# Performance work log

Hardware: AMD Instinct MI355X
Metric: run time of the kernel (lower is better)

## Reference

```python
import jax, jax.numpy as jnp
import numpy as np


def log_g(x):
    # log of g(x) = x + 0.5 for x>=0, sigmoid(x) for x<0
    return jnp.where(x >= 0, jnp.log(jax.nn.relu(x) + 0.5), -jax.nn.softplus(-x))


def setup_inputs() -> dict:
    key = jax.random.key(0)
    k1, k2 = jax.random.split(key)
    B, S, D = 4, 4096, 1024
    x = jax.random.normal(k1, (B, S, D), dtype=jnp.float32)
    # nn.Linear(dim, 2*dim, bias=False) weight: [2*dim, dim], scaled like kaiming-uniform-ish
    W = jax.random.normal(k2, (2 * D, D), dtype=jnp.float32) * (1.0 / np.sqrt(D))
    return {"x": x, "W": W}


def reference(x, W):
    # x: [B, S, D], W: [2D, D] -> hidden, gate: [B, S, D]
    hg = jnp.einsum("bsd,ed->bse", x, W)
    hidden, gate = jnp.split(hg, 2, axis=-1)

    log_coeffs = -jax.nn.softplus(gate)        # log(1 - z)
    log_z = -jax.nn.softplus(-gate)            # log(z)
    log_values = log_z + log_g(hidden)

    # Heinsen associative scan in log space along seq axis
    a_star = jnp.cumsum(log_coeffs, axis=1)
    log_h0_plus_b_star = jax.lax.cumlogsumexp(log_values - a_star, axis=1)
    log_h = a_star + log_h0_plus_b_star
    out = jnp.exp(log_h)                       # [B, S, D]
    # expansion_factor == 1.0 -> to_out is Identity
    return out
```

## Files before the change

kernel.cpp:

```cpp
#include <hip/hip_runtime.h>
#include <hip/hip_bf16.h>
#include <hip/hip_fp16.h>
#include <math.h>
#include <string.h>

#define B_  4
#define S_  4096
#define D_  1024
#define M_  (B_ * S_)
#define K_  D_
#define L_  32
#define NC_ (S_ / L_)
#define NKT 16

typedef __attribute__((ext_vector_type(8))) short          bf16x8;
typedef __attribute__((ext_vector_type(8))) unsigned short u16x8;
typedef __attribute__((ext_vector_type(4))) float          f32x4;

__device__ __forceinline__ unsigned short f2bf(float f) {
    union { __hip_bfloat16 h; unsigned short u; } cv;
    cv.h = __float2bfloat16(f);
    return cv.u;
}

__device__ __forceinline__ float fast_rcp(float x) {
#if __has_builtin(__builtin_amdgcn_rcpf)
    return __builtin_amdgcn_rcpf(x);
#else
    return 1.0f / x;
#endif
}

__device__ __forceinline__ void stage16(const unsigned short* src, char* dst) {
    __builtin_amdgcn_global_load_lds(
        (const __attribute__((address_space(1))) unsigned int*)src,
        (__attribute__((address_space(3))) unsigned int*)dst, 16, 0, 0);
}

__global__ __launch_bounds__(256) void to_bf16_both(
    const float* __restrict__ x, const float* __restrict__ W,
    unsigned short* __restrict__ xb, unsigned short* __restrict__ Wb,
    int n8x, int n8w)
{
    int i = blockIdx.x * 256 + threadIdx.x;
    const float* src;
    unsigned short* dst;
    int j;
    if (i < n8x) { src = x; dst = xb; j = i; }
    else {
        j = i - n8x;
        if (j >= n8w) return;
        src = W; dst = Wb;
    }
    const float4* p = (const float4*)src + (size_t)j * 2;
    float4 a = p[0], b = p[1];
    u16x8 o;
    o[0] = f2bf(a.x); o[1] = f2bf(a.y); o[2] = f2bf(a.z); o[3] = f2bf(a.w);
    o[4] = f2bf(b.x); o[5] = f2bf(b.y); o[6] = f2bf(b.z); o[7] = f2bf(b.w);
    *(u16x8*)(dst + (size_t)j * 8) = o;
}

__global__ __launch_bounds__(512, 2) void gemm_pointwise(
    const unsigned short* __restrict__ xb, const unsigned short* __restrict__ Wb,
    __half2* __restrict__ cvb, float2* __restrict__ CVagg)
{
    __shared__ char lds[131072];

    const int th   = threadIdx.x;
    const int lane = th & 63;
    const int wave = th >> 6;
    const int wm = wave >> 2;
    const int wn = wave & 3;

    const int wg  = blockIdx.x;
    const int swz = (wg & 7) * 64 + (wg >> 3);
    const int m0 = (swz >> 3) * 256;
    const int d0 = (swz & 7) * 128;

    f32x4 acc[8][4];
#pragma unroll
    for (int i = 0; i < 8; ++i)
#pragma unroll
        for (int j = 0; j < 4; ++j)
            acc[i][j] = (f32x4){0.f, 0.f, 0.f, 0.f};

    const int srow = th >> 2;
    const int scol = (((th & 3) ^ ((th >> 3) & 3)) * 8);
    const unsigned short* srcA  = xb + (size_t)(m0 + srow)       * K_ + scol;
    const unsigned short* srcA2 = xb + (size_t)(m0 + 128 + srow) * K_ + scol;
    const unsigned short* srcBh = Wb + (size_t)(d0 + srow)       * K_ + scol;
    const unsigned short* srcBg = Wb + (size_t)(D_ + d0 + srow)  * K_ + scol;
    char* const wuo = lds + wave * 1024;

    const int lr = lane & 15;
    const int lq = lane >> 4;
    const int lkb = ((lq ^ ((lr >> 1) & 3)) * 16);
    const int aoffb = (wm * 128 + lr) * 64 + lkb;
    const int boffb = 32768 + (wn * 32 + lr) * 64 + lkb;

    bf16x8 Aa[4], Ab[4], Ba[4], Bb[4];

#define BAR()  asm volatile("s_barrier" ::: "memory")
#define LGK0() asm volatile("s_waitcnt lgkmcnt(0)" ::: "memory")
#define VM0()  asm volatile("s_waitcnt vmcnt(0)" ::: "memory")

#define CLUSTER(base, AF, BF) do {                                        \
    __builtin_amdgcn_s_setprio(1);                                        \
    _Pragma("unroll")                                                     \
    for (int i_ = 0; i_ < 4; ++i_)                                        \
        _Pragma("unroll")                                                 \
        for (int j_ = 0; j_ < 4; ++j_)                                    \
            acc[(base) + i_][j_] = __builtin_amdgcn_mfma_f32_16x16x32_bf16(\
                AF[i_], BF[j_], acc[(base) + i_][j_], 0, 0, 0);           \
    __builtin_amdgcn_s_setprio(0);                                        \
  } while (0)

    stage16(srcA,       wuo + 0);
    stage16(srcA2,      wuo + 8192);
    stage16(srcA  + 32, wuo + 16384);
    stage16(srcA2 + 32, wuo + 24576);
    stage16(srcBh,      wuo + 32768);
    stage16(srcBg,      wuo + 40960);
    stage16(srcBh + 32, wuo + 49152);
    stage16(srcBg + 32, wuo + 57344);
    VM0();
    BAR();
    {
        const char* bc = lds;
#pragma unroll
        for (int i = 0; i < 4; ++i)
            Aa[i] = *(const bf16x8*)(bc + aoffb + i * 1024);
#pragma unroll
        for (int j = 0; j < 2; ++j) {
            Ba[j]     = *(const bf16x8*)(bc + boffb + j * 1024);
            Ba[j + 2] = *(const bf16x8*)(bc + boffb + 8192 + j * 1024);
        }
    }

#pragma unroll 1
    for (int t = 0; t < NKT; ++t) {
        const char* bc  = lds + (t & 1) * 65536;
        char*       bn  = wuo + ((t + 1) & 1) * 65536;
        const char* bnr = lds + ((t + 1) & 1) * 65536;
        const int kof = (t + 1) * 64;
        const bool pre = (t < NKT - 1);

#pragma unroll
        for (int i = 0; i < 4; ++i)
            Ab[i] = *(const bf16x8*)(bc + aoffb + 4096 + i * 1024);
        if (pre) {
            stage16(srcA  + kof,      bn + 0);
            stage16(srcA2 + kof,      bn + 8192);
            stage16(srcA  + kof + 32, bn + 16384);
            stage16(srcA2 + kof + 32, bn + 24576);
        }
        BAR(); LGK0();
        CLUSTER(0, Aa, Ba);
        BAR();

#pragma unroll
        for (int i = 0; i < 4; ++i)
            Aa[i] = *(const bf16x8*)(bc + aoffb + 16384 + i * 1024);
#pragma unroll
        for (int j = 0; j < 2; ++j) {
            Bb[j]     = *(const bf16x8*)(bc + boffb + 16384 + j * 1024);
            Bb[j + 2] = *(const bf16x8*)(bc + boffb + 16384 + 8192 + j * 1024);
        }
        if (pre) {
            stage16(srcBh + kof,      bn + 32768);
            stage16(srcBg + kof,      bn + 40960);
            stage16(srcBh + kof + 32, bn + 49152);
            stage16(srcBg + kof + 32, bn + 57344);
        }
        BAR(); LGK0();
        CLUSTER(4, Ab, Ba);
        BAR();

#pragma unroll
        for (int i = 0; i < 4; ++i)
            Ab[i] = *(const bf16x8*)(bc + aoffb + 4096 + 16384 + i * 1024);
        BAR(); LGK0();
        CLUSTER(0, Aa, Bb);
        BAR();

        VM0();
        BAR();
        if (pre) {
#pragma unroll
            for (int i = 0; i < 4; ++i)
                Aa[i] = *(const bf16x8*)(bnr + aoffb + i * 1024);
#pragma unroll
            for (int j = 0; j < 2; ++j) {
                Ba[j]     = *(const bf16x8*)(bnr + boffb + j * 1024);
                Ba[j + 2] = *(const bf16x8*)(bnr + boffb + 8192 + j * 1024);
            }
        }
        CLUSTER(4, Ab, Bb);
    }
#undef CLUSTER
#undef BAR
#undef LGK0
#undef VM0

#pragma unroll
    for (int mp = 0; mp < 4; ++mp) {
        float C16[2][2], V16[2][2];
#pragma unroll
        for (int hf = 0; hf < 2; ++hf) {
            const int mi = mp * 2 + hf;
#pragma unroll
            for (int nj = 0; nj < 2; ++nj) {
                float C4 = 1.0f, V4 = 0.0f;
                const int d = d0 + wn * 32 + nj * 16 + lr;
#pragma unroll
                for (int r = 0; r < 4; ++r) {
                    int m = m0 + wm * 128 + mi * 16 + lq * 4 + r;
                    float h = acc[mi][nj][r];
                    float g = acc[mi][nj + 2][r];
                    float eg  = __expf(g);
                    float c   = fast_rcp(1.0f + eg);
                    float z   = eg * c;
                    float enh = __expf(-h);
                    float sh  = fast_rcp(1.0f + enh);
                    float gh  = (h >= 0.0f) ? (h + 0.5f) : sh;
                    float v   = z * gh;
                    cvb[(size_t)m * D_ + d] = __floats2half2_rn(c, v);
                    V4 = fmaf(c, V4, v);
                    C4 *= c;
                }
                float Ca = __shfl_xor(C4, 16), Va = __shfl_xor(V4, 16);
                float Clo = (lq & 1) ? Ca : C4, Vlo = (lq & 1) ? Va : V4;
                float Chi = (lq & 1) ? C4 : Ca, Vhi = (lq & 1) ? V4 : Va;
                float C2 = Clo * Chi, V2 = fmaf(Chi, Vlo, Vhi);
                float Cb = __shfl_xor(C2, 32), Vb = __shfl_xor(V2, 32);
                float Cl2 = (lq & 2) ? Cb : C2, Vl2 = (lq & 2) ? Vb : V2;
                float Ch2 = (lq & 2) ? C2 : Cb, Vh2 = (lq & 2) ? V2 : Vb;
                C16[hf][nj] = Cl2 * Ch2;
                V16[hf][nj] = fmaf(Ch2, Vl2, Vh2);
            }
        }
        if (lq == 0) {
            const int chunkg = (m0 + wm * 128 + mp * 32) >> 5;
#pragma unroll
            for (int nj = 0; nj < 2; ++nj) {
                float C32 = C16[0][nj] * C16[1][nj];
                float V32 = fmaf(C16[1][nj], V16[0][nj], V16[1][nj]);
                const int d = d0 + wn * 32 + nj * 16 + lr;
                float2 st; st.x = C32; st.y = V32;
                CVagg[(size_t)chunkg * D_ + d] = st;
            }
        }
    }
}

__global__ __launch_bounds__(256) void chunk_scan(
    const float2* __restrict__ CVagg, float* __restrict__ P)
{
    const int d = blockIdx.x * 256 + threadIdx.x;
    const int b = blockIdx.z;
    float h = 0.0f;
    for (int c = 0; c < NC_; ++c) {
        size_t o = ((size_t)b * NC_ + c) * D_ + d;
        P[o] = h;
        float2 cv = CVagg[o];
        h = fmaf(cv.x, h, cv.y);
    }
}

__global__ __launch_bounds__(256) void chunk_apply(
    const unsigned long long* __restrict__ cvw,
    const float* __restrict__ P, float* __restrict__ out)
{
    const int d = (blockIdx.x * 256 + threadIdx.x) * 2;
    const int c = blockIdx.y;
    const int b = blockIdx.z;
    size_t base2 = (((size_t)(b * S_ + c * L_)) * D_ + d) >> 1;
    float2 h2 = *(const float2*)(P + ((size_t)b * NC_ + c) * D_ + d);
    float h0 = h2.x, h1 = h2.y;
    unsigned long long* outp = (unsigned long long*)out;
    union Cvt { unsigned long long ull; uint2 u2; float2 f2; };
#pragma unroll
    for (int s = 0; s < L_; ++s) {
        Cvt in;
        in.ull = __builtin_nontemporal_load(cvw + base2 + (size_t)s * (D_ / 2));
        float2 p0 = __half22float2(*(const __half2*)&in.u2.x);
        float2 p1 = __half22float2(*(const __half2*)&in.u2.y);
        h0 = fmaf(p0.x, h0, p0.y);
        h1 = fmaf(p1.x, h1, p1.y);
        Cvt o;
        o.f2.x = h0; o.f2.y = h1;
        __builtin_nontemporal_store(o.ull, outp + base2 + (size_t)s * (D_ / 2));
    }
}

extern "C" void kernel_launch(void* const* d_in, const int* in_sizes, int n_in,
                              void* d_out, int out_size, void* d_ws, size_t ws_size,
                              hipStream_t stream) {
    const float* x = (const float*)d_in[0];
    const float* W = (const float*)d_in[1];
    float* out = (float*)d_out;

    float2* CVagg = (float2*)d_ws;
    float*  P     = (float*)(CVagg + (size_t)B_ * NC_ * D_);
    __half2* cvb  = (__half2*)(P + (size_t)B_ * NC_ * D_);
    unsigned short* xb = (unsigned short*)(cvb + (size_t)M_ * D_);
    unsigned short* Wb = xb + (size_t)M_ * K_;

    const int n8x = M_ * K_ / 8;
    const int n8w = 2 * D_ * K_ / 8;
    to_bf16_both<<<(n8x + n8w + 255) / 256, 256, 0, stream>>>(x, W, xb, Wb, n8x, n8w);

    gemm_pointwise<<<512, 512, 0, stream>>>(xb, Wb, cvb, CVagg);

    dim3 g3(D_ / 256, 1, B_);
    chunk_scan<<<g3, 256, 0, stream>>>(CVagg, P);

    dim3 g2(D_ / 512, NC_, B_);
    chunk_apply<<<g2, 256, 0, stream>>>((const unsigned long long*)cvb, P, out);
}
```

Measured before the change: 123.8 us.

## Fuse x fp32-to-bf16 conversion into GEMM A-tile loading via registers

After: 126.3 us. +2.0%, slower.

```diff
diff --git a/kernel.cpp b/kernel.cpp
--- a/kernel.cpp
+++ b/kernel.cpp
@@ -2,7 +2,6 @@
 #include <hip/hip_bf16.h>
 #include <hip/hip_fp16.h>
 #include <math.h>
-#include <string.h>
 
 #define B_  4
 #define S_  4096
@@ -37,31 +36,21 @@
         (__attribute__((address_space(3))) unsigned int*)dst, 16, 0, 0);
 }
 
-__global__ __launch_bounds__(256) void to_bf16_both(
-    const float* __restrict__ x, const float* __restrict__ W,
-    unsigned short* __restrict__ xb, unsigned short* __restrict__ Wb,
-    int n8x, int n8w)
+__global__ __launch_bounds__(256) void to_bf16(
+    const float* __restrict__ in, unsigned short* __restrict__ out, int n8)
 {
     int i = blockIdx.x * 256 + threadIdx.x;
-    const float* src;
-    unsigned short* dst;
-    int j;
-    if (i < n8x) { src = x; dst = xb; j = i; }
-    else {
-        j = i - n8x;
-        if (j >= n8w) return;
-        src = W; dst = Wb;
-    }
-    const float4* p = (const float4*)src + (size_t)j * 2;
+    if (i >= n8) return;
+    const float4* p = (const float4*)in + (size_t)i * 2;
     float4 a = p[0], b = p[1];
     u16x8 o;
     o[0] = f2bf(a.x); o[1] = f2bf(a.y); o[2] = f2bf(a.z); o[3] = f2bf(a.w);
     o[4] = f2bf(b.x); o[5] = f2bf(b.y); o[6] = f2bf(b.z); o[7] = f2bf(b.w);
-    *(u16x8*)(dst + (size_t)j * 8) = o;
+    *(u16x8*)(out + (size_t)i * 8) = o;
 }
 
 __global__ __launch_bounds__(512, 2) void gemm_pointwise(
-    const unsigned short* __restrict__ xb, const unsigned short* __restrict__ Wb,
+    const float* __restrict__ xf, const unsigned short* __restrict__ Wb,
     __half2* __restrict__ cvb, float2* __restrict__ CVagg)
 {
     __shared__ char lds[131072];
@@ -86,11 +75,12 @@
 
     const int srow = th >> 2;
     const int scol = (((th & 3) ^ ((th >> 3) & 3)) * 8);
-    const unsigned short* srcA  = xb + (size_t)(m0 + srow)       * K_ + scol;
-    const unsigned short* srcA2 = xb + (size_t)(m0 + 128 + srow) * K_ + scol;
-    const unsigned short* srcBh = Wb + (size_t)(d0 + srow)       * K_ + scol;
-    const unsigned short* srcBg = Wb + (size_t)(D_ + d0 + srow)  * K_ + scol;
+    const float*          srcAf  = xf + (size_t)(m0 + srow)       * K_ + scol;
+    const float*          srcAf2 = xf + (size_t)(m0 + 128 + srow) * K_ + scol;
+    const unsigned short* srcBh  = Wb + (size_t)(d0 + srow)       * K_ + scol;
+    const unsigned short* srcBg  = Wb + (size_t)(D_ + d0 + srow)  * K_ + scol;
     char* const wuo = lds + wave * 1024;
+    const int thb = th * 16;
 
     const int lr = lane & 15;
     const int lq = lane >> 4;
@@ -99,10 +89,39 @@
     const int boffb = 32768 + (wn * 32 + lr) * 64 + lkb;
 
     bf16x8 Aa[4], Ab[4], Ba[4], Bb[4];
+    float4 aL[8];
 
 #define BAR()  asm volatile("s_barrier" ::: "memory")
 #define LGK0() asm volatile("s_waitcnt lgkmcnt(0)" ::: "memory")
 #define VM0()  asm volatile("s_waitcnt vmcnt(0)" ::: "memory")
+
+#define LOAD_A(kof) do {                                                  \
+    const float* s0_ = srcAf  + (kof);                                    \
+    const float* s1_ = srcAf2 + (kof);                                    \
+    aL[0] = *(const float4*)(s0_);      aL[1] = *(const float4*)(s0_ + 4);\
+    aL[2] = *(const float4*)(s1_);      aL[3] = *(const float4*)(s1_ + 4);\
+    aL[4] = *(const float4*)(s0_ + 32); aL[5] = *(const float4*)(s0_ + 36);\
+    aL[6] = *(const float4*)(s1_ + 32); aL[7] = *(const float4*)(s1_ + 36);\
+  } while (0)
+
+#define WRITE_A(dst) do {                                                 \
+    _Pragma("unroll")                                                     \
+    for (int s_ = 0; s_ < 4; ++s_) {                                      \
+        u16x8 o_;                                                         \
+        o_[0] = f2bf(aL[2*s_].x);   o_[1] = f2bf(aL[2*s_].y);             \
+        o_[2] = f2bf(aL[2*s_].z);   o_[3] = f2bf(aL[2*s_].w);             \
+        o_[4] = f2bf(aL[2*s_+1].x); o_[5] = f2bf(aL[2*s_+1].y);           \
+        o_[6] = f2bf(aL[2*s_+1].z); o_[7] = f2bf(aL[2*s_+1].w);           \
+        *(u16x8*)((dst) + s_ * 8192 + thb) = o_;                          \
+    }                                                                     \
+  } while (0)
+
+#define STAGE_B(kof, bufdst) do {                                         \
+    stage16(srcBh + (kof),      (bufdst) + 32768);                        \
+    stage16(srcBg + (kof),      (bufdst) + 40960);                        \
+    stage16(srcBh + (kof) + 32, (bufdst) + 49152);                        \
+    stage16(srcBg + (kof) + 32, (bufdst) + 57344);                        \
+  } while (0)
 
 #define CLUSTER(base, AF, BF) do {                                        \
     __builtin_amdgcn_s_setprio(1);                                        \
@@ -115,15 +134,11 @@
     __builtin_amdgcn_s_setprio(0);                                        \
   } while (0)
 
-    stage16(srcA,       wuo + 0);
-    stage16(srcA2,      wuo + 8192);
-    stage16(srcA  + 32, wuo + 16384);
-    stage16(srcA2 + 32, wuo + 24576);
-    stage16(srcBh,      wuo + 32768);
-    stage16(srcBg,      wuo + 40960);
-    stage16(srcBh + 32, wuo + 49152);
-    stage16(srcBg + 32, wuo + 57344);
+    LOAD_A(0);
+    STAGE_B(0, wuo);
     VM0();
+    WRITE_A(lds);
+    LGK0();
     BAR();
     {
         const char* bc = lds;
@@ -141,6 +156,7 @@
     for (int t = 0; t < NKT; ++t) {
         const char* bc  = lds + (t & 1) * 65536;
         char*       bn  = wuo + ((t + 1) & 1) * 65536;
+        char*       bnw = lds + ((t + 1) & 1) * 65536;
         const char* bnr = lds + ((t + 1) & 1) * 65536;
         const int kof = (t + 1) * 64;
         const bool pre = (t < NKT - 1);
@@ -148,12 +164,7 @@
 #pragma unroll
         for (int i = 0; i < 4; ++i)
             Ab[i] = *(const bf16x8*)(bc + aoffb + 4096 + i * 1024);
-        if (pre) {
-            stage16(srcA  + kof,      bn + 0);
-            stage16(srcA2 + kof,      bn + 8192);
-            stage16(srcA  + kof + 32, bn + 16384);
-            stage16(srcA2 + kof + 32, bn + 24576);
-        }
+        if (pre) { LOAD_A(kof); }
         BAR(); LGK0();
         CLUSTER(0, Aa, Ba);
         BAR();
@@ -166,12 +177,7 @@
             Bb[j]     = *(const bf16x8*)(bc + boffb + 16384 + j * 1024);
             Bb[j + 2] = *(const bf16x8*)(bc + boffb + 16384 + 8192 + j * 1024);
         }
-        if (pre) {
-            stage16(srcBh + kof,      bn + 32768);
-            stage16(srcBg + kof,      bn + 40960);
-            stage16(srcBh + kof + 32, bn + 49152);
-            stage16(srcBg + kof + 32, bn + 57344);
-        }
+        if (pre) { STAGE_B(kof, bn); }
         BAR(); LGK0();
         CLUSTER(4, Ab, Ba);
         BAR();
@@ -184,6 +190,8 @@
         BAR();
 
         VM0();
+        if (pre) { WRITE_A(bnw); }
+        LGK0();
         BAR();
         if (pre) {
 #pragma unroll
@@ -198,6 +206,9 @@
         CLUSTER(4, Ab, Bb);
     }
 #undef CLUSTER
+#undef STAGE_B
+#undef WRITE_A
+#undef LOAD_A
 #undef BAR
 #undef LGK0
 #undef VM0
@@ -303,14 +314,12 @@
     float2* CVagg = (float2*)d_ws;
     float*  P     = (float*)(CVagg + (size_t)B_ * NC_ * D_);
     __half2* cvb  = (__half2*)(P + (size_t)B_ * NC_ * D_);
-    unsigned short* xb = (unsigned short*)(cvb + (size_t)M_ * D_);
-    unsigned short* Wb = xb + (size_t)M_ * K_;
-
-    const int n8x = M_ * K_ / 8;
+    unsigned short* Wb = (unsigned short*)(cvb + (size_t)M_ * D_);
+
     const int n8w = 2 * D_ * K_ / 8;
-    to_bf16_both<<<(n8x + n8w + 255) / 256, 256, 0, stream>>>(x, W, xb, Wb, n8x, n8w);
-
-    gemm_pointwise<<<512, 512, 0, stream>>>(xb, Wb, cvb, CVagg);
+    to_bf16<<<(n8w + 255) / 256, 256, 0, stream>>>(W, Wb, n8w);
+
+    gemm_pointwise<<<512, 512, 0, stream>>>(x, Wb, cvb, CVagg);
 
     dim3 g3(D_ / 256, 1, B_);
     chunk_scan<<<g3, 256, 0, stream>>>(CVagg, P);
```

## Load B fragments directly from global memory, staging only A in LDS

Applied to the files above, without the earlier changes.

Result: slower. 167.1 us (+34.9%).

```diff
diff --git a/kernel.cpp b/kernel.cpp
--- a/kernel.cpp
+++ b/kernel.cpp
@@ -2,7 +2,6 @@
 #include <hip/hip_bf16.h>
 #include <hip/hip_fp16.h>
 #include <math.h>
-#include <string.h>
 
 #define B_  4
 #define S_  4096
@@ -64,7 +63,7 @@
     const unsigned short* __restrict__ xb, const unsigned short* __restrict__ Wb,
     __half2* __restrict__ cvb, float2* __restrict__ CVagg)
 {
-    __shared__ char lds[131072];
+    __shared__ char lds[65536];
 
     const int th   = threadIdx.x;
     const int lane = th & 63;
@@ -88,21 +87,41 @@
     const int scol = (((th & 3) ^ ((th >> 3) & 3)) * 8);
     const unsigned short* srcA  = xb + (size_t)(m0 + srow)       * K_ + scol;
     const unsigned short* srcA2 = xb + (size_t)(m0 + 128 + srow) * K_ + scol;
-    const unsigned short* srcBh = Wb + (size_t)(d0 + srow)       * K_ + scol;
-    const unsigned short* srcBg = Wb + (size_t)(D_ + d0 + srow)  * K_ + scol;
     char* const wuo = lds + wave * 1024;
 
     const int lr = lane & 15;
     const int lq = lane >> 4;
     const int lkb = ((lq ^ ((lr >> 1) & 3)) * 16);
     const int aoffb = (wm * 128 + lr) * 64 + lkb;
-    const int boffb = 32768 + (wn * 32 + lr) * 64 + lkb;
+
+    const unsigned short* bhp = Wb + (size_t)(d0 + wn * 32 + lr) * K_ + lq * 8;
+    const unsigned short* bgp = bhp + (size_t)D_ * K_;
 
     bf16x8 Aa[4], Ab[4], Ba[4], Bb[4];
 
 #define BAR()  asm volatile("s_barrier" ::: "memory")
 #define LGK0() asm volatile("s_waitcnt lgkmcnt(0)" ::: "memory")
 #define VM0()  asm volatile("s_waitcnt vmcnt(0)" ::: "memory")
+
+#define STAGE_A(kof, bufdst) do {                                         \
+    stage16(srcA  + (kof),      (bufdst) + 0);                            \
+    stage16(srcA2 + (kof),      (bufdst) + 8192);                         \
+    stage16(srcA  + (kof) + 32, (bufdst) + 16384);                        \
+    stage16(srcA2 + (kof) + 32, (bufdst) + 24576);                        \
+  } while (0)
+
+#define LOAD_BA(tt) do { const int kc_ = (tt) * 64;                       \
+    Ba[0] = *(const bf16x8*)(bhp + kc_);                                  \
+    Ba[1] = *(const bf16x8*)(bhp + 16 * K_ + kc_);                        \
+    Ba[2] = *(const bf16x8*)(bgp + kc_);                                  \
+    Ba[3] = *(const bf16x8*)(bgp + 16 * K_ + kc_);                        \
+  } while (0)
+#define LOAD_BB(tt) do { const int kc_ = (tt) * 64 + 32;                  \
+    Bb[0] = *(const bf16x8*)(bhp + kc_);                                  \
+    Bb[1] = *(const bf16x8*)(bhp + 16 * K_ + kc_);                        \
+    Bb[2] = *(const bf16x8*)(bgp + kc_);                                  \
+    Bb[3] = *(const bf16x8*)(bgp + 16 * K_ + kc_);                        \
+  } while (0)
 
 #define CLUSTER(base, AF, BF) do {                                        \
     __builtin_amdgcn_s_setprio(1);                                        \
@@ -115,45 +134,27 @@
     __builtin_amdgcn_s_setprio(0);                                        \
   } while (0)
 
-    stage16(srcA,       wuo + 0);
-    stage16(srcA2,      wuo + 8192);
-    stage16(srcA  + 32, wuo + 16384);
-    stage16(srcA2 + 32, wuo + 24576);
-    stage16(srcBh,      wuo + 32768);
-    stage16(srcBg,      wuo + 40960);
-    stage16(srcBh + 32, wuo + 49152);
-    stage16(srcBg + 32, wuo + 57344);
+    STAGE_A(0, wuo);
+    LOAD_BA(0);
     VM0();
     BAR();
-    {
-        const char* bc = lds;
-#pragma unroll
-        for (int i = 0; i < 4; ++i)
-            Aa[i] = *(const bf16x8*)(bc + aoffb + i * 1024);
-#pragma unroll
-        for (int j = 0; j < 2; ++j) {
-            Ba[j]     = *(const bf16x8*)(bc + boffb + j * 1024);
-            Ba[j + 2] = *(const bf16x8*)(bc + boffb + 8192 + j * 1024);
-        }
-    }
+#pragma unroll
+    for (int i = 0; i < 4; ++i)
+        Aa[i] = *(const bf16x8*)(lds + aoffb + i * 1024);
 
 #pragma unroll 1
     for (int t = 0; t < NKT; ++t) {
-        const char* bc  = lds + (t & 1) * 65536;
-        char*       bn  = wuo + ((t + 1) & 1) * 65536;
-        const char* bnr = lds + ((t + 1) & 1) * 65536;
+        const char* bc  = lds + (t & 1) * 32768;
+        char*       bn  = wuo + ((t + 1) & 1) * 32768;
+        const char* bnr = lds + ((t + 1) & 1) * 32768;
         const int kof = (t + 1) * 64;
         const bool pre = (t < NKT - 1);
 
 #pragma unroll
         for (int i = 0; i < 4; ++i)
             Ab[i] = *(const bf16x8*)(bc + aoffb + 4096 + i * 1024);
-        if (pre) {
-            stage16(srcA  + kof,      bn + 0);
-            stage16(srcA2 + kof,      bn + 8192);
-            stage16(srcA  + kof + 32, bn + 16384);
-            stage16(srcA2 + kof + 32, bn + 24576);
-        }
+        if (pre) { STAGE_A(kof, bn); }
+        LOAD_BB(t);
         BAR(); LGK0();
         CLUSTER(0, Aa, Ba);
         BAR();
@@ -161,17 +162,6 @@
 #pragma unroll
         for (int i = 0; i < 4; ++i)
             Aa[i] = *(const bf16x8*)(bc + aoffb + 16384 + i * 1024);
-#pragma unroll
-        for (int j = 0; j < 2; ++j) {
-            Bb[j]     = *(const bf16x8*)(bc + boffb + 16384 + j * 1024);
-            Bb[j + 2] = *(const bf16x8*)(bc + boffb + 16384 + 8192 + j * 1024);
-        }
-        if (pre) {
-            stage16(srcBh + kof,      bn + 32768);
-            stage16(srcBg + kof,      bn + 40960);
-            stage16(srcBh + kof + 32, bn + 49152);
-            stage16(srcBg + kof + 32, bn + 57344);
-        }
         BAR(); LGK0();
         CLUSTER(4, Ab, Ba);
         BAR();
@@ -186,18 +176,17 @@
         VM0();
         BAR();
         if (pre) {
+            LOAD_BA(t + 1);
 #pragma unroll
             for (int i = 0; i < 4; ++i)
                 Aa[i] = *(const bf16x8*)(bnr + aoffb + i * 1024);
-#pragma unroll
-            for (int j = 0; j < 2; ++j) {
-                Ba[j]     = *(const bf16x8*)(bnr + boffb + j * 1024);
-                Ba[j + 2] = *(const bf16x8*)(bnr + boffb + 8192 + j * 1024);
-            }
         }
         CLUSTER(4, Ab, Bb);
     }
 #undef CLUSTER
+#undef LOAD_BA
+#undef LOAD_BB
+#undef STAGE_A
 #undef BAR
 #undef LGK0
 #undef VM0
```
